# Kernel tuning notes

Hardware: AMD Instinct MI355X
Metric: run time of the kernel (lower is better)

Reference implementation:

```python
import jax, jax.numpy as jnp
import numpy as np

D_MODEL = 1024
D_PROJ = D_MODEL // 4


def setup_inputs() -> dict:
    key = jax.random.key(0)
    k1, k2, k3 = jax.random.split(key, 3)
    hidden_states = jax.random.normal(k1, (4, 2048, D_MODEL), dtype=jnp.float32)
    proj_w = jax.random.normal(k2, (D_PROJ, D_MODEL), dtype=jnp.float32) * 0.02
    proj_b = jnp.zeros((D_PROJ,), dtype=jnp.float32)
    clf_w = jax.random.normal(k3, (1, 1), dtype=jnp.float32) * 0.02
    clf_b = jnp.zeros((1,), dtype=jnp.float32)
    return {"hidden_states": hidden_states, "proj_w": proj_w, "proj_b": proj_b,
            "clf_w": clf_w, "clf_b": clf_b}


def reference(hidden_states, proj_w, proj_b, clf_w, clf_b):
    # h: [B, S, D/4]
    h = jax.nn.relu(jnp.einsum('bsd,pd->bsp', hidden_states, proj_w) + proj_b)
    # pairwise dot products == batched h @ h^T: [B, S, S]
    scores = jnp.einsum('bip,bjp->bij', h, h)
    # scalar affine classifier (Linear(1,1)) folded in
    return scores * clf_w[0, 0] + clf_b[0]
```

## Files before the change

### kernel.cpp

```cpp
#include <hip/hip_runtime.h>
#include <hip/hip_bf16.h>

typedef __bf16 bf16_t;
typedef __attribute__((ext_vector_type(8))) __bf16 bf16x8;
typedef __attribute__((ext_vector_type(4))) float f32x4;

#define SEQ    2048
#define DMODEL 1024
#define DPROJ  256
#define NBATCH 4

__device__ __forceinline__ bf16x8 cvt8(const float4& lo, const float4& hi) {
    bf16x8 v;
    v[0] = (bf16_t)lo.x; v[1] = (bf16_t)lo.y; v[2] = (bf16_t)lo.z; v[3] = (bf16_t)lo.w;
    v[4] = (bf16_t)hi.x; v[5] = (bf16_t)hi.y; v[6] = (bf16_t)hi.z; v[7] = (bf16_t)hi.w;
    return v;
}

__device__ __forceinline__ void gl_lds16(const void* g, void* l) {
    __builtin_amdgcn_global_load_lds(
        (const __attribute__((address_space(1))) unsigned int*)g,
        (__attribute__((address_space(3))) unsigned int*)l, 16, 0, 0);
}

__global__ __launch_bounds__(256) void proj_kernel(
    const float* __restrict__ X, const float* __restrict__ W,
    const float* __restrict__ bias, bf16_t* __restrict__ H)
{
    __shared__ __align__(16) bf16_t Xs[64 * 64];
    __shared__ __align__(16) bf16_t Ws[64 * 64];

    const int m0 = blockIdx.x * 64;
    const int n0 = blockIdx.y * 64;
    const int tid  = threadIdx.x;
    const int lane = tid & 63;
    const int wave = tid >> 6;
    const int quad = lane >> 4;
    const int l16  = lane & 15;
    const int wm = (wave & 1) * 32;
    const int wn = (wave >> 1) * 32;
    const int swz = l16 & 7;

    int srow[2], scol[2];
    bf16_t* lx[2];
    bf16_t* lw[2];
    #pragma unroll
    for (int r = 0; r < 2; ++r) {
        const int p = r * 256 + tid;
        srow[r] = p >> 3;
        scol[r] = p & 7;
        const int cs = (scol[r] ^ (srow[r] & 7)) * 8;
        lx[r] = Xs + srow[r] * 64 + cs;
        lw[r] = Ws + srow[r] * 64 + cs;
    }

    float4 xr[2][2][2], wr[2][2][2];

    #pragma unroll
    for (int s = 0; s < 2; ++s) {
        const int k0 = s * 64;
        #pragma unroll
        for (int r = 0; r < 2; ++r) {
            const float* gx = X + (size_t)(m0 + srow[r]) * DMODEL + k0 + scol[r] * 8;
            xr[s][r][0] = *(const float4*)gx;
            xr[s][r][1] = *(const float4*)(gx + 4);
            const float* gw = W + (size_t)(n0 + srow[r]) * DMODEL + k0 + scol[r] * 8;
            wr[s][r][0] = *(const float4*)gw;
            wr[s][r][1] = *(const float4*)(gw + 4);
        }
    }

    f32x4 acc[2][2] = {};

    #pragma unroll
    for (int kt = 0; kt < 16; ++kt) {
        const int s = kt & 1;
        __syncthreads();
        #pragma unroll
        for (int r = 0; r < 2; ++r) {
            *(bf16x8*)lx[r] = cvt8(xr[s][r][0], xr[s][r][1]);
            *(bf16x8*)lw[r] = cvt8(wr[s][r][0], wr[s][r][1]);
        }
        __syncthreads();

        if (kt < 14) {
            const int k0 = (kt + 2) * 64;
            #pragma unroll
            for (int r = 0; r < 2; ++r) {
                const float* gx = X + (size_t)(m0 + srow[r]) * DMODEL + k0 + scol[r] * 8;
                xr[s][r][0] = *(const float4*)gx;
                xr[s][r][1] = *(const float4*)(gx + 4);
                const float* gw = W + (size_t)(n0 + srow[r]) * DMODEL + k0 + scol[r] * 8;
                wr[s][r][0] = *(const float4*)gw;
                wr[s][r][1] = *(const float4*)(gw + 4);
            }
        }

        #pragma unroll
        for (int ks = 0; ks < 2; ++ks) {
            bf16x8 af[2], bfr[2];
            #pragma unroll
            for (int i = 0; i < 2; ++i) {
                const int ch = (((ks << 2) | quad) ^ swz) * 8;
                af[i]  = *(const bf16x8*)&Xs[(wm + i * 16 + l16) * 64 + ch];
                bfr[i] = *(const bf16x8*)&Ws[(wn + i * 16 + l16) * 64 + ch];
            }
            #pragma unroll
            for (int i = 0; i < 2; ++i)
                #pragma unroll
                for (int j = 0; j < 2; ++j)
                    acc[i][j] = __builtin_amdgcn_mfma_f32_16x16x32_bf16(
                        af[i], bfr[j], acc[i][j], 0, 0, 0);
        }
    }

    #pragma unroll
    for (int i = 0; i < 2; ++i) {
        #pragma unroll
        for (int j = 0; j < 2; ++j) {
            const int gn = n0 + wn + j * 16 + l16;
            const float bv = bias[gn];
            #pragma unroll
            for (int r = 0; r < 4; ++r) {
                const int gm = m0 + wm + i * 16 + quad * 4 + r;
                float v = acc[i][j][r] + bv;
                v = v > 0.f ? v : 0.f;
                H[(size_t)gm * DPROJ + gn] = (bf16_t)v;
            }
        }
    }
}

__global__ __launch_bounds__(512) void score_kernel(
    const bf16_t* __restrict__ H, const float* __restrict__ clf_w,
    const float* __restrict__ clf_b, float* __restrict__ Out)
{
    __shared__ __align__(16) bf16_t As[128 * 64];
    __shared__ __align__(16) bf16_t Bs[128 * 64];

    int t = blockIdx.x, bi = 0, rl = SEQ / 128;
    while (t >= rl) { t -= rl; --rl; ++bi; }
    const int bj = bi + t;
    const int b  = blockIdx.y;
    const int m0 = bi * 128;
    const int n0 = bj * 128;
    const bf16_t* Hb = H + (size_t)b * SEQ * DPROJ;
    float* Ob = Out + (size_t)b * SEQ * SEQ;

    const int tid  = threadIdx.x;
    const int lane = tid & 63;
    const int wave = tid >> 6;
    const int quad = lane >> 4;
    const int l16  = lane & 15;
    const int wm = (wave & 3) * 32;
    const int wn = (wave >> 2) * 64;
    const int swz = l16 & 7;

    const bf16_t* gA[2];
    const bf16_t* gB[2];
    bf16_t* lA[2];
    bf16_t* lB[2];
    #pragma unroll
    for (int t2 = 0; t2 < 2; ++t2) {
        const int g   = (wave * 2 + t2) * 64 + lane;
        const int row = g >> 3;
        const int gc  = (g & 7) ^ (row & 7);
        gA[t2] = Hb + (size_t)(m0 + row) * DPROJ + gc * 8;
        gB[t2] = Hb + (size_t)(n0 + row) * DPROJ + gc * 8;
        lA[t2] = As + (wave * 2 + t2) * 512;
        lB[t2] = Bs + (wave * 2 + t2) * 512;
    }

    f32x4 acc[2][4] = {};

    for (int kt = 0; kt < 4; ++kt) {
        __syncthreads();
        #pragma unroll
        for (int t2 = 0; t2 < 2; ++t2) {
            gl_lds16(gA[t2], lA[t2]);
            gl_lds16(gB[t2], lB[t2]);
        }
        __syncthreads();
        #pragma unroll
        for (int t2 = 0; t2 < 2; ++t2) { gA[t2] += 64; gB[t2] += 64; }

        #pragma unroll
        for (int ks = 0; ks < 2; ++ks) {
            const int ch = (((ks << 2) | quad) ^ swz) * 8;
            bf16x8 af[2], bfr[4];
            #pragma unroll
            for (int i = 0; i < 2; ++i)
                af[i] = *(const bf16x8*)&As[(wm + i * 16 + l16) * 64 + ch];
            #pragma unroll
            for (int j = 0; j < 4; ++j)
                bfr[j] = *(const bf16x8*)&Bs[(wn + j * 16 + l16) * 64 + ch];
            #pragma unroll
            for (int i = 0; i < 2; ++i)
                #pragma unroll
                for (int j = 0; j < 4; ++j)
                    acc[i][j] = __builtin_amdgcn_mfma_f32_16x16x32_bf16(
                        af[i], bfr[j], acc[i][j], 0, 0, 0);
        }
    }

    const float scale = clf_w[0];
    const float off   = clf_b[0];

    #pragma unroll
    for (int i = 0; i < 2; ++i)
        #pragma unroll
        for (int j = 0; j < 4; ++j)
            #pragma unroll
            for (int r = 0; r < 4; ++r) {
                const int gm = m0 + wm + i * 16 + quad * 4 + r;
                const int gn = n0 + wn + j * 16 + l16;
                Ob[(size_t)gm * SEQ + gn] = acc[i][j][r] * scale + off;
            }

    if (bi != bj) {
        #pragma unroll
        for (int i = 0; i < 2; ++i)
            #pragma unroll
            for (int j = 0; j < 4; ++j) {
                const int gn = n0 + wn + j * 16 + l16;
                const int gm = m0 + wm + i * 16 + quad * 4;
                float4 v;
                v.x = acc[i][j][0] * scale + off;
                v.y = acc[i][j][1] * scale + off;
                v.z = acc[i][j][2] * scale + off;
                v.w = acc[i][j][3] * scale + off;
                *(float4*)&Ob[(size_t)gn * SEQ + gm] = v;
            }
    }
}

extern "C" void kernel_launch(void* const* d_in, const int* in_sizes, int n_in,
                              void* d_out, int out_size, void* d_ws, size_t ws_size,
                              hipStream_t stream) {
    const float* X    = (const float*)d_in[0];
    const float* W    = (const float*)d_in[1];
    const float* bias = (const float*)d_in[2];
    const float* clfw = (const float*)d_in[3];
    const float* clfb = (const float*)d_in[4];
    float* Out = (float*)d_out;
    bf16_t* H  = (bf16_t*)d_ws;

    dim3 g1(NBATCH * SEQ / 64, DPROJ / 64, 1);
    proj_kernel<<<g1, 256, 0, stream>>>(X, W, bias, H);

    const int ntile = SEQ / 128;
    dim3 g2(ntile * (ntile + 1) / 2, NBATCH);
    score_kernel<<<g2, 512, 0, stream>>>(H, clfw, clfb, Out);
}
```

Baseline: 123.7 us.

## Pre-convert projection weights to bf16 and load MFMA fragments directly from global

Adds a small kernel that converts the fp32 projection weight to bf16 once into workspace, then rewrites the projection GEMM to drop LDS staging. Each lane loads its own MFMA fragment straight from global memory (fp32 X converted in registers, bf16 W), with a two-step register prefetch. This removes the LDS stores, loads and barriers, and halves weight read traffic. In exchange, each X element is now read from global by several waves with no LDS reuse, relying on the cache, and there is an extra kernel launch.

New measurement: 148.8 us. 20.3% more time.

```diff
diff --git a/kernel.cpp b/kernel.cpp
--- a/kernel.cpp
+++ b/kernel.cpp
@@ -23,13 +23,19 @@
         (__attribute__((address_space(3))) unsigned int*)l, 16, 0, 0);
 }
 
+__global__ __launch_bounds__(256) void wcvt_kernel(
+    const float* __restrict__ W, bf16_t* __restrict__ Wb)
+{
+    const int idx = (blockIdx.x * 256 + threadIdx.x) * 8;
+    float4 lo = *(const float4*)(W + idx);
+    float4 hi = *(const float4*)(W + idx + 4);
+    *(bf16x8*)(Wb + idx) = cvt8(lo, hi);
+}
+
 __global__ __launch_bounds__(256) void proj_kernel(
-    const float* __restrict__ X, const float* __restrict__ W,
+    const float* __restrict__ X, const bf16_t* __restrict__ Wb,
     const float* __restrict__ bias, bf16_t* __restrict__ H)
 {
-    __shared__ __align__(16) bf16_t Xs[64 * 64];
-    __shared__ __align__(16) bf16_t Ws[64 * 64];
-
     const int m0 = blockIdx.x * 64;
     const int n0 = blockIdx.y * 64;
     const int tid  = threadIdx.x;
@@ -39,72 +45,56 @@
     const int l16  = lane & 15;
     const int wm = (wave & 1) * 32;
     const int wn = (wave >> 1) * 32;
-    const int swz = l16 & 7;
-
-    int srow[2], scol[2];
-    bf16_t* lx[2];
-    bf16_t* lw[2];
-    #pragma unroll
-    for (int r = 0; r < 2; ++r) {
-        const int p = r * 256 + tid;
-        srow[r] = p >> 3;
-        scol[r] = p & 7;
-        const int cs = (scol[r] ^ (srow[r] & 7)) * 8;
-        lx[r] = Xs + srow[r] * 64 + cs;
-        lw[r] = Ws + srow[r] * 64 + cs;
-    }
-
-    float4 xr[2][2][2], wr[2][2][2];
-
+
+    const float*  xrow[2];
+    const bf16_t* wrow[2];
+    #pragma unroll
+    for (int i = 0; i < 2; ++i)
+        xrow[i] = X + (size_t)(m0 + wm + i * 16 + l16) * DMODEL + quad * 8;
+    #pragma unroll
+    for (int j = 0; j < 2; ++j)
+        wrow[j] = Wb + (size_t)(n0 + wn + j * 16 + l16) * DMODEL + quad * 8;
+
+    float4 xs[2][2][2];
+    bf16x8 wf[2][2];
     #pragma unroll
     for (int s = 0; s < 2; ++s) {
-        const int k0 = s * 64;
-        #pragma unroll
-        for (int r = 0; r < 2; ++r) {
-            const float* gx = X + (size_t)(m0 + srow[r]) * DMODEL + k0 + scol[r] * 8;
-            xr[s][r][0] = *(const float4*)gx;
-            xr[s][r][1] = *(const float4*)(gx + 4);
-            const float* gw = W + (size_t)(n0 + srow[r]) * DMODEL + k0 + scol[r] * 8;
-            wr[s][r][0] = *(const float4*)gw;
-            wr[s][r][1] = *(const float4*)(gw + 4);
-        }
+        #pragma unroll
+        for (int i = 0; i < 2; ++i) {
+            xs[s][i][0] = *(const float4*)(xrow[i] + s * 32);
+            xs[s][i][1] = *(const float4*)(xrow[i] + s * 32 + 4);
+        }
+        #pragma unroll
+        for (int j = 0; j < 2; ++j)
+            wf[s][j] = *(const bf16x8*)(wrow[j] + s * 32);
     }
 
     f32x4 acc[2][2] = {};
 
-    #pragma unroll
-    for (int kt = 0; kt < 16; ++kt) {
-        const int s = kt & 1;
-        __syncthreads();
-        #pragma unroll
-        for (int r = 0; r < 2; ++r) {
-            *(bf16x8*)lx[r] = cvt8(xr[s][r][0], xr[s][r][1]);
-            *(bf16x8*)lw[r] = cvt8(wr[s][r][0], wr[s][r][1]);
-        }
-        __syncthreads();
-
-        if (kt < 14) {
-            const int k0 = (kt + 2) * 64;
-            #pragma unroll
-            for (int r = 0; r < 2; ++r) {
-                const float* gx = X + (size_t)(m0 + srow[r]) * DMODEL + k0 + scol[r] * 8;
-                xr[s][r][0] = *(const float4*)gx;
-                xr[s][r][1] = *(const float4*)(gx + 4);
-                const float* gw = W + (size_t)(n0 + srow[r]) * DMODEL + k0 + scol[r] * 8;
-                wr[s][r][0] = *(const float4*)gw;
-                wr[s][r][1] = *(const float4*)(gw + 4);
-            }
-        }
-
-        #pragma unroll
-        for (int ks = 0; ks < 2; ++ks) {
+    for (int kk = 0; kk < 16; ++kk) {
+        #pragma unroll
+        for (int s = 0; s < 2; ++s) {
+            const int step = kk * 2 + s;
             bf16x8 af[2], bfr[2];
             #pragma unroll
-            for (int i = 0; i < 2; ++i) {
-                const int ch = (((ks << 2) | quad) ^ swz) * 8;
-                af[i]  = *(const bf16x8*)&Xs[(wm + i * 16 + l16) * 64 + ch];
-                bfr[i] = *(const bf16x8*)&Ws[(wn + i * 16 + l16) * 64 + ch];
-            }
+            for (int i = 0; i < 2; ++i)
+                af[i] = cvt8(xs[s][i][0], xs[s][i][1]);
+            #pragma unroll
+            for (int j = 0; j < 2; ++j)
+                bfr[j] = wf[s][j];
+
+            if (step < 30) {
+                const int k = (step + 2) * 32;
+                #pragma unroll
+                for (int i = 0; i < 2; ++i) {
+                    xs[s][i][0] = *(const float4*)(xrow[i] + k);
+                    xs[s][i][1] = *(const float4*)(xrow[i] + k + 4);
+                }
+                #pragma unroll
+                for (int j = 0; j < 2; ++j)
+                    wf[s][j] = *(const bf16x8*)(wrow[j] + k);
+            }
+
             #pragma unroll
             for (int i = 0; i < 2; ++i)
                 #pragma unroll
@@ -244,9 +234,12 @@
     const float* clfb = (const float*)d_in[4];
     float* Out = (float*)d_out;
     bf16_t* H  = (bf16_t*)d_ws;
+    bf16_t* Wb = (bf16_t*)d_ws + (size_t)8192 * DPROJ;
+
+    wcvt_kernel<<<DPROJ * DMODEL / (256 * 8), 256, 0, stream>>>(W, Wb);
 
     dim3 g1(NBATCH * SEQ / 64, DPROJ / 64, 1);
-    proj_kernel<<<g1, 256, 0, stream>>>(X, W, bias, H);
+    proj_kernel<<<g1, 256, 0, stream>>>(X, Wb, bias, H);
 
     const int ntile = SEQ / 128;
     dim3 g2(ntile * (ntile + 1) / 2, NBATCH);
```
